# Performance work log

Hardware: AMD Instinct MI355X
Metric: run time of the kernel (lower is better)

The kernel has to match this reference:

```python
import jax, jax.numpy as jnp
import numpy as np

B, S, D, H = 2, 2048, 1024, 16
HD = D // H  # head_dim = 64


def setup_inputs() -> dict:
    key = jax.random.key(0)
    ks = jax.random.split(key, 11)
    init = 1.0 / np.sqrt(D)
    inp = {
        "query": jax.random.normal(ks[0], (B, S, D), jnp.float32),
        "key": jax.random.normal(ks[1], (B, S, D), jnp.float32),
        "value": jax.random.normal(ks[2], (B, S, D), jnp.float32),
        "Wq": jax.random.uniform(ks[3], (D, D), jnp.float32, -init, init),
        "bq": jax.random.uniform(ks[4], (D,), jnp.float32, -init, init),
        "Wk": jax.random.uniform(ks[5], (D, D), jnp.float32, -init, init),
        "bk": jax.random.uniform(ks[6], (D,), jnp.float32, -init, init),
        "Wv": jax.random.uniform(ks[7], (D, D), jnp.float32, -init, init),
        "bv": jax.random.uniform(ks[8], (D,), jnp.float32, -init, init),
        "Wo": jax.random.uniform(ks[9], (D, D), jnp.float32, -init, init),
        "bo": jax.random.uniform(ks[10], (D,), jnp.float32, -init, init),
    }
    return inp


def reference(query, key, value, Wq, bq, Wk, bk, Wv, bv, Wo, bo):
    # Linear projections (torch Linear: x @ W.T + b)
    q = query @ Wq.T + bq  # [B,S,D]
    k = key @ Wk.T + bk
    v = value @ Wv.T + bv
    # split heads -> [B,H,S,HD]
    q = q.reshape(B, S, H, HD).transpose(0, 2, 1, 3)
    k = k.reshape(B, S, H, HD).transpose(0, 2, 1, 3)
    v = v.reshape(B, S, H, HD).transpose(0, 2, 1, 3)
    # NOTE: original code divides by scale = head_dim**-0.5, i.e. multiplies
    # scores by sqrt(head_dim). Reproduced faithfully.
    scale = HD ** (-0.5)
    scores = jnp.einsum("bhqd,bhkd->bhqk", q, k) / scale  # [B,H,S,S]
    attn = jax.nn.softmax(scores, axis=-1)
    x = jnp.einsum("bhqk,bhkd->bhqd", attn, v)  # [B,H,S,HD]
    x = x.transpose(0, 2, 1, 3).reshape(B, S, D)
    return x @ Wo.T + bo
```

## Files before the change

### kernel.cpp

```cpp
#include <hip/hip_runtime.h>
#include <stdint.h>
#include <stddef.h>

#define SCALE_LOG2E 11.541560327111707f
#define E8 4194304
#define M1 1048576

typedef __attribute__((ext_vector_type(8))) _Float16 f16x8;
typedef __attribute__((ext_vector_type(4))) _Float16 f16x4;
typedef __attribute__((ext_vector_type(4))) float f32x4;

#if __has_builtin(__builtin_amdgcn_exp2f)
#define EXP2F(x) __builtin_amdgcn_exp2f(x)
#else
#define EXP2F(x) exp2f(x)
#endif

__device__ __forceinline__ f32x4 mfma_f16(f16x8 a, f16x8 b, f32x4 c) {
  return __builtin_amdgcn_mfma_f32_16x16x32_f16(a, b, c, 0, 0, 0);
}

__device__ __forceinline__ void async16(const void* g, void* lds) {
  __builtin_amdgcn_global_load_lds(
      (const __attribute__((address_space(1))) unsigned int*)g,
      (__attribute__((address_space(3))) unsigned int*)lds, 16, 0, 0);
}

__global__ void prep_x(const float* __restrict__ q, const float* __restrict__ k,
                       const float* __restrict__ v, _Float16* __restrict__ dst) {
  const int i = blockIdx.x * 256 + threadIdx.x;
  const int z = blockIdx.y;
  const float* s = (z == 0) ? q : (z == 1) ? k : v;
  float4 x = ((const float4*)s)[i];
  f16x4 h = {(_Float16)x.x, (_Float16)x.y, (_Float16)x.z, (_Float16)x.w};
  ((f16x4*)(dst + (size_t)z * E8))[i] = h;
}

__global__ void prep_w4(const float* __restrict__ wq, const float* __restrict__ wk,
                        const float* __restrict__ wv, const float* __restrict__ wo,
                        _Float16* __restrict__ dst) {
  const int i = blockIdx.x * 256 + threadIdx.x;
  const int z = blockIdx.y;
  const float* s = (z == 0) ? wq : (z == 1) ? wk : (z == 2) ? wv : wo;
  float4 x = ((const float4*)s)[i];
  f16x4 h = {(_Float16)x.x, (_Float16)x.y, (_Float16)x.z, (_Float16)x.w};
  ((f16x4*)(dst + (size_t)z * M1))[i] = h;
}

__global__ __launch_bounds__(256) void gemm_qkv(
    const _Float16* __restrict__ Xf,
    const _Float16* __restrict__ Wf,
    const float* __restrict__ bq, const float* __restrict__ bk,
    const float* __restrict__ bv,
    _Float16* __restrict__ Of)
{
  __shared__ _Float16 LA[4096];
  __shared__ _Float16 LB[4096];
  const int z = blockIdx.z;
  const int tid = threadIdx.x;
  const int lane = tid & 63;
  const int wv = tid >> 6;
  const int wm = wv >> 1, wn = wv & 1;
  const int rl = lane & 15, qd = lane >> 4;
  const int m0 = blockIdx.y * 128, n0 = blockIdx.x * 128;

  const _Float16* A0 = Xf + (size_t)z * E8;
  const _Float16* W0 = Wf + (size_t)z * M1;
  const float* bias = (z == 0) ? bq : (z == 1) ? bk : bv;

  f32x4 acc[4][4];
#pragma unroll
  for (int i = 0; i < 4; i++)
#pragma unroll
    for (int j = 0; j < 4; j++) acc[i][j] = f32x4{0.f, 0.f, 0.f, 0.f};

  const int srow = wv * 32 + (lane >> 2);
  const int scol = (lane & 3) * 8;

  for (int k0 = 0; k0 < 1024; k0 += 32) {
    const _Float16* ga = A0 + (size_t)(m0 + srow) * 1024 + k0 + scol;
    async16(ga, &LA[wv * 1024]);
    async16(ga + 16 * 1024, &LA[wv * 1024 + 512]);
    const _Float16* gb = W0 + (size_t)(n0 + srow) * 1024 + k0 + scol;
    async16(gb, &LB[wv * 1024]);
    async16(gb + 16 * 1024, &LB[wv * 1024 + 512]);
    __syncthreads();
    f16x8 af[4], bfr[4];
#pragma unroll
    for (int i = 0; i < 4; i++) af[i] = *(const f16x8*)&LA[(wm * 64 + i * 16 + rl) * 32 + qd * 8];
#pragma unroll
    for (int j = 0; j < 4; j++) bfr[j] = *(const f16x8*)&LB[(wn * 64 + j * 16 + rl) * 32 + qd * 8];
#pragma unroll
    for (int i = 0; i < 4; i++)
#pragma unroll
      for (int j = 0; j < 4; j++) acc[i][j] = mfma_f16(af[i], bfr[j], acc[i][j]);
    __syncthreads();
  }

  if (z == 2) {
#pragma unroll
    for (int j = 0; j < 4; j++) {
      const int nn = n0 + wn * 64 + j * 16 + rl;
      const float bj = bias[nn];
      const int hh = nn >> 6, e = nn & 63;
#pragma unroll
      for (int i = 0; i < 4; i++) {
        const int mm = m0 + wm * 64 + i * 16 + qd * 4;
        const int b = mm >> 11, s = mm & 2047;
        f16x4 pk = {(_Float16)(acc[i][j][0] + bj), (_Float16)(acc[i][j][1] + bj),
                    (_Float16)(acc[i][j][2] + bj), (_Float16)(acc[i][j][3] + bj)};
        *(f16x4*)(Of + 2 * (size_t)E8 + (((size_t)((b * 16 + hh) * 64 + e)) << 11) + s) = pk;
      }
    }
  } else {
    const float scl = (z == 0) ? SCALE_LOG2E : 1.0f;
    _Float16* base = Of + (size_t)z * E8;
#pragma unroll
    for (int j = 0; j < 4; j++) {
      const int nn = n0 + wn * 64 + j * 16 + rl;
      const float bj = bias[nn];
      const int hh = nn >> 6, e = nn & 63;
#pragma unroll
      for (int i = 0; i < 4; i++) {
        const int mm = m0 + wm * 64 + i * 16 + qd * 4;
        const int b = mm >> 11;
#pragma unroll
        for (int r = 0; r < 4; r++) {
          const int s = (mm + r) & 2047;
          base[((size_t)((b * 16 + hh) * 2048 + s) << 6) + e] =
              (_Float16)((acc[i][j][r] + bj) * scl);
        }
      }
    }
  }
}

__global__ __launch_bounds__(256, 2) void attn_kernel(
    const _Float16* __restrict__ Qb,
    const _Float16* __restrict__ Kb,
    const _Float16* __restrict__ Vt,
    _Float16* __restrict__ Xo)
{
  __shared__ _Float16 Ks[2][4096];
  __shared__ _Float16 Vs[2][4096];
  __shared__ _Float16 Ps[4][32][76];
  const int tid = threadIdx.x;
  const int lane = tid & 63;
  const int wv = tid >> 6;
  const int rl = lane & 15, qd = lane >> 4;
  const int bh = blockIdx.y;
  const int q0 = blockIdx.x * 128 + wv * 32;

  f16x8 qf[2][2];
#pragma unroll
  for (int mt = 0; mt < 2; mt++)
#pragma unroll
    for (int kk = 0; kk < 2; kk++)
      qf[mt][kk] = *(const f16x8*)(Qb + ((size_t)bh * 2048 + q0 + mt * 16 + rl) * 64 +
                                   kk * 32 + qd * 8);

  float m_[2] = {-1e30f, -1e30f}, l_[2] = {0.f, 0.f};
  f32x4 o[2][4];
#pragma unroll
  for (int mt = 0; mt < 2; mt++)
#pragma unroll
    for (int jt = 0; jt < 4; jt++) o[mt][jt] = f32x4{0.f, 0.f, 0.f, 0.f};

  auto stage = [&](int kv, int buf) {
#pragma unroll
    for (int it = 0; it < 2; it++) {
      const int cI = it * 256 + tid;
      const int row = cI >> 3;
      const int c = (cI & 7) ^ (row & 7);
      const int dst = (it * 256 + wv * 64) * 8;
      async16(Kb + ((size_t)bh * 2048 + kv + row) * 64 + c * 8, &Ks[buf][dst]);
      async16(Vt + ((size_t)bh * 64 + row) * 2048 + kv + c * 8, &Vs[buf][dst]);
    }
  };

  stage(0, 0);

  for (int t = 0; t < 32; t++) {
    const int buf = t & 1;
    __syncthreads();
    if (t + 1 < 32) stage((t + 1) * 64, buf ^ 1);

    f32x4 sc[2][4];
#pragma unroll
    for (int mt = 0; mt < 2; mt++)
#pragma unroll
      for (int nt = 0; nt < 4; nt++) sc[mt][nt] = f32x4{0.f, 0.f, 0.f, 0.f};
#pragma unroll
    for (int nt = 0; nt < 4; nt++) {
      const int ro = (nt * 16 + rl) * 64;
#pragma unroll
      for (int kk = 0; kk < 2; kk++) {
        const int cc = (((kk * 4 + qd) ^ (rl & 7)) << 3);
        f16x8 kh = *(const f16x8*)&Ks[buf][ro + cc];
#pragma unroll
        for (int mt = 0; mt < 2; mt++)
          sc[mt][nt] = mfma_f16(kh, qf[mt][kk], sc[mt][nt]);
      }
    }

#pragma unroll
    for (int mt = 0; mt < 2; mt++) {
      float mx = sc[mt][0][0];
#pragma unroll
      for (int nt = 0; nt < 4; nt++)
#pragma unroll
        for (int r = 0; r < 4; r++) mx = fmaxf(mx, sc[mt][nt][r]);
      mx = fmaxf(mx, __shfl_xor(mx, 16));
      mx = fmaxf(mx, __shfl_xor(mx, 32));
      const float mold = m_[mt];
      const float mnew = fmaxf(mold, mx);
      m_[mt] = mnew;
      float sm = 0.f;
#pragma unroll
      for (int nt = 0; nt < 4; nt++)
#pragma unroll
        for (int r = 0; r < 4; r++) {
          float p = EXP2F(sc[mt][nt][r] - mnew);
          sc[mt][nt][r] = p;
          sm += p;
        }
      sm += __shfl_xor(sm, 16);
      sm += __shfl_xor(sm, 32);
      if (__any(mnew > mold)) {
        const float al = EXP2F(mold - mnew);
        l_[mt] = l_[mt] * al + sm;
#pragma unroll
        for (int jt = 0; jt < 4; jt++)
#pragma unroll
          for (int r = 0; r < 4; r++) o[mt][jt][r] *= al;
      } else {
        l_[mt] += sm;
      }

#pragma unroll
      for (int nt = 0; nt < 4; nt++) {
        f16x4 pk = {(_Float16)sc[mt][nt][0], (_Float16)sc[mt][nt][1],
                    (_Float16)sc[mt][nt][2], (_Float16)sc[mt][nt][3]};
        *(f16x4*)&Ps[wv][mt * 16 + rl][nt * 16 + qd * 4] = pk;
      }
    }

#pragma unroll
    for (int kk2 = 0; kk2 < 2; kk2++) {
      f16x8 pf[2];
#pragma unroll
      for (int mt = 0; mt < 2; mt++)
        pf[mt] = *(const f16x8*)&Ps[wv][mt * 16 + rl][kk2 * 32 + qd * 8];
#pragma unroll
      for (int jt = 0; jt < 4; jt++) {
        const int cc = (((kk2 * 4 + qd) ^ (rl & 7)) << 3);
        f16x8 vv = *(const f16x8*)&Vs[buf][(jt * 16 + rl) * 64 + cc];
#pragma unroll
        for (int mt = 0; mt < 2; mt++)
          o[mt][jt] = mfma_f16(vv, pf[mt], o[mt][jt]);
      }
    }
  }

  const int b = bh >> 4, hh = bh & 15;
#pragma unroll
  for (int mt = 0; mt < 2; mt++) {
    const float inv = 1.0f / l_[mt];
    const int q = q0 + mt * 16 + rl;
#pragma unroll
    for (int jt = 0; jt < 4; jt++) {
      f16x4 pk = {(_Float16)(o[mt][jt][0] * inv), (_Float16)(o[mt][jt][1] * inv),
                  (_Float16)(o[mt][jt][2] * inv), (_Float16)(o[mt][jt][3] * inv)};
      *(f16x4*)(Xo + ((size_t)(b * 2048 + q)) * 1024 + hh * 64 + jt * 16 + qd * 4) = pk;
    }
  }
}

__global__ __launch_bounds__(256) void gemm_out(
    const _Float16* __restrict__ A0,
    const _Float16* __restrict__ W0,
    const float* __restrict__ bias,
    float* __restrict__ out)
{
  __shared__ _Float16 LA[4096];
  __shared__ _Float16 LB[4096];
  const int tid = threadIdx.x;
  const int lane = tid & 63;
  const int wv = tid >> 6;
  const int wm = wv >> 1, wn = wv & 1;
  const int rl = lane & 15, qd = lane >> 4;
  const int m0 = blockIdx.y * 128, n0 = blockIdx.x * 128;

  f32x4 acc[4][4];
#pragma unroll
  for (int i = 0; i < 4; i++)
#pragma unroll
    for (int j = 0; j < 4; j++) acc[i][j] = f32x4{0.f, 0.f, 0.f, 0.f};

  const int srow = wv * 32 + (lane >> 2);
  const int scol = (lane & 3) * 8;

  for (int k0 = 0; k0 < 1024; k0 += 32) {
    const _Float16* ga = A0 + (size_t)(m0 + srow) * 1024 + k0 + scol;
    async16(ga, &LA[wv * 1024]);
    async16(ga + 16 * 1024, &LA[wv * 1024 + 512]);
    const _Float16* gb = W0 + (size_t)(n0 + srow) * 1024 + k0 + scol;
    async16(gb, &LB[wv * 1024]);
    async16(gb + 16 * 1024, &LB[wv * 1024 + 512]);
    __syncthreads();
    f16x8 af[4], bfr[4];
#pragma unroll
    for (int i = 0; i < 4; i++) af[i] = *(const f16x8*)&LA[(wm * 64 + i * 16 + rl) * 32 + qd * 8];
#pragma unroll
    for (int j = 0; j < 4; j++) bfr[j] = *(const f16x8*)&LB[(wn * 64 + j * 16 + rl) * 32 + qd * 8];
#pragma unroll
    for (int i = 0; i < 4; i++)
#pragma unroll
      for (int j = 0; j < 4; j++) acc[i][j] = mfma_f16(af[i], bfr[j], acc[i][j]);
    __syncthreads();
  }

#pragma unroll
  for (int j = 0; j < 4; j++) {
    const int nn = n0 + wn * 64 + j * 16 + rl;
    const float bj = bias[nn];
#pragma unroll
    for (int i = 0; i < 4; i++) {
      const int mm = m0 + wm * 64 + i * 16 + qd * 4;
#pragma unroll
      for (int r = 0; r < 4; r++)
        out[(size_t)(mm + r) * 1024 + nn] = acc[i][j][r] + bj;
    }
  }
}

extern "C" void kernel_launch(void* const* d_in, const int* in_sizes, int n_in,
                              void* d_out, int out_size, void* d_ws, size_t ws_size,
                              hipStream_t stream) {
  const float* query = (const float*)d_in[0];
  const float* key   = (const float*)d_in[1];
  const float* value = (const float*)d_in[2];
  const float* Wq = (const float*)d_in[3];
  const float* bq = (const float*)d_in[4];
  const float* Wk = (const float*)d_in[5];
  const float* bk = (const float*)d_in[6];
  const float* Wv = (const float*)d_in[7];
  const float* bv = (const float*)d_in[8];
  const float* Wo = (const float*)d_in[9];
  const float* bo = (const float*)d_in[10];

  _Float16* ws = (_Float16*)d_ws;
  _Float16* Xf = ws;
  _Float16* Wf = ws + 3 * (size_t)E8;
  _Float16* Qh = Wf + 4 * (size_t)M1;
  _Float16* Kh = Qh + (size_t)E8;
  _Float16* Vt = Kh + (size_t)E8;
  _Float16* Xa = Vt + (size_t)E8;

  prep_x<<<dim3(4096, 3), 256, 0, stream>>>(query, key, value, Xf);
  prep_w4<<<dim3(1024, 4), 256, 0, stream>>>(Wq, Wk, Wv, Wo, Wf);

  gemm_qkv<<<dim3(8, 32, 3), 256, 0, stream>>>(Xf, Wf, bq, bk, bv, Qh);
  attn_kernel<<<dim3(16, 32), 256, 0, stream>>>(Qh, Kh, Vt, Xa);
  gemm_out<<<dim3(8, 32), 256, 0, stream>>>(Xa, Wf + 3 * (size_t)M1, bo, (float*)d_out);
}
```

Measured before the change: 259.7 us.

## Double-buffer GEMMs, halve attention and out-proj tiles, merge prep kernels

Merges the two fp16 conversion kernels into one launch. Adds double-buffered LDS staging with a single barrier per k-step to both GEMMs. Halves the attention query tile per wave (16 rows), which doubles the grid, and switches to a per-lane local-max softmax with the row sum reduced only at the end. Shrinks the output-projection M tile to 64 so more blocks run. The aim is to hide global-load latency and raise occupancy and block count. The cost is more K/V reloads per query in attention and somewhat different fp16 rounding of the probabilities.

```diff
diff --git a/kernel.cpp b/kernel.cpp
--- a/kernel.cpp
+++ b/kernel.cpp
@@ -26,36 +26,41 @@
       (__attribute__((address_space(3))) unsigned int*)lds, 16, 0, 0);
 }
 
-__global__ void prep_x(const float* __restrict__ q, const float* __restrict__ k,
-                       const float* __restrict__ v, _Float16* __restrict__ dst) {
-  const int i = blockIdx.x * 256 + threadIdx.x;
-  const int z = blockIdx.y;
-  const float* s = (z == 0) ? q : (z == 1) ? k : v;
-  float4 x = ((const float4*)s)[i];
+__global__ void prep_all(const float* __restrict__ q, const float* __restrict__ k,
+                         const float* __restrict__ v,
+                         const float* __restrict__ wq, const float* __restrict__ wk,
+                         const float* __restrict__ wv, const float* __restrict__ wo,
+                         _Float16* __restrict__ Xf, _Float16* __restrict__ Wf) {
+  const int gid = blockIdx.x;
+  const float* src;
+  _Float16* dst;
+  int i;
+  if (gid < 12288) {
+    const int z = gid >> 12;
+    src = (z == 0) ? q : (z == 1) ? k : v;
+    dst = Xf + (size_t)z * E8;
+    i = (gid & 4095) * 256 + threadIdx.x;
+  } else {
+    const int g2 = gid - 12288;
+    const int z = g2 >> 10;
+    src = (z == 0) ? wq : (z == 1) ? wk : (z == 2) ? wv : wo;
+    dst = Wf + (size_t)z * M1;
+    i = (g2 & 1023) * 256 + threadIdx.x;
+  }
+  float4 x = ((const float4*)src)[i];
   f16x4 h = {(_Float16)x.x, (_Float16)x.y, (_Float16)x.z, (_Float16)x.w};
-  ((f16x4*)(dst + (size_t)z * E8))[i] = h;
-}
-
-__global__ void prep_w4(const float* __restrict__ wq, const float* __restrict__ wk,
-                        const float* __restrict__ wv, const float* __restrict__ wo,
-                        _Float16* __restrict__ dst) {
-  const int i = blockIdx.x * 256 + threadIdx.x;
-  const int z = blockIdx.y;
-  const float* s = (z == 0) ? wq : (z == 1) ? wk : (z == 2) ? wv : wo;
-  float4 x = ((const float4*)s)[i];
-  f16x4 h = {(_Float16)x.x, (_Float16)x.y, (_Float16)x.z, (_Float16)x.w};
-  ((f16x4*)(dst + (size_t)z * M1))[i] = h;
-}
-
-__global__ __launch_bounds__(256) void gemm_qkv(
+  ((f16x4*)dst)[i] = h;
+}
+
+__global__ __launch_bounds__(256, 3) void gemm_qkv(
     const _Float16* __restrict__ Xf,
     const _Float16* __restrict__ Wf,
     const float* __restrict__ bq, const float* __restrict__ bk,
     const float* __restrict__ bv,
     _Float16* __restrict__ Of)
 {
-  __shared__ _Float16 LA[4096];
-  __shared__ _Float16 LB[4096];
+  __shared__ _Float16 LA[2][4096];
+  __shared__ _Float16 LB[2][4096];
   const int z = blockIdx.z;
   const int tid = threadIdx.x;
   const int lane = tid & 63;
@@ -77,24 +82,29 @@
   const int srow = wv * 32 + (lane >> 2);
   const int scol = (lane & 3) * 8;
 
-  for (int k0 = 0; k0 < 1024; k0 += 32) {
+  auto stage = [&](int k0, int buf) {
     const _Float16* ga = A0 + (size_t)(m0 + srow) * 1024 + k0 + scol;
-    async16(ga, &LA[wv * 1024]);
-    async16(ga + 16 * 1024, &LA[wv * 1024 + 512]);
+    async16(ga, &LA[buf][wv * 1024]);
+    async16(ga + 16 * 1024, &LA[buf][wv * 1024 + 512]);
     const _Float16* gb = W0 + (size_t)(n0 + srow) * 1024 + k0 + scol;
-    async16(gb, &LB[wv * 1024]);
-    async16(gb + 16 * 1024, &LB[wv * 1024 + 512]);
+    async16(gb, &LB[buf][wv * 1024]);
+    async16(gb + 16 * 1024, &LB[buf][wv * 1024 + 512]);
+  };
+
+  stage(0, 0);
+  for (int t = 0; t < 32; t++) {
+    const int buf = t & 1;
     __syncthreads();
+    if (t + 1 < 32) stage((t + 1) * 32, buf ^ 1);
     f16x8 af[4], bfr[4];
 #pragma unroll
-    for (int i = 0; i < 4; i++) af[i] = *(const f16x8*)&LA[(wm * 64 + i * 16 + rl) * 32 + qd * 8];
-#pragma unroll
-    for (int j = 0; j < 4; j++) bfr[j] = *(const f16x8*)&LB[(wn * 64 + j * 16 + rl) * 32 + qd * 8];
+    for (int i = 0; i < 4; i++) af[i] = *(const f16x8*)&LA[buf][(wm * 64 + i * 16 + rl) * 32 + qd * 8];
+#pragma unroll
+    for (int j = 0; j < 4; j++) bfr[j] = *(const f16x8*)&LB[buf][(wn * 64 + j * 16 + rl) * 32 + qd * 8];
 #pragma unroll
     for (int i = 0; i < 4; i++)
 #pragma unroll
       for (int j = 0; j < 4; j++) acc[i][j] = mfma_f16(af[i], bfr[j], acc[i][j]);
-    __syncthreads();
   }
 
   if (z == 2) {
@@ -135,7 +145,7 @@
   }
 }
 
-__global__ __launch_bounds__(256, 2) void attn_kernel(
+__global__ __launch_bounds__(256, 3) void attn_kernel(
     const _Float16* __restrict__ Qb,
     const _Float16* __restrict__ Kb,
     const _Float16* __restrict__ Vt,
@@ -143,28 +153,23 @@
 {
   __shared__ _Float16 Ks[2][4096];
   __shared__ _Float16 Vs[2][4096];
-  __shared__ _Float16 Ps[4][32][76];
+  __shared__ _Float16 Ps[4][16][76];
   const int tid = threadIdx.x;
   const int lane = tid & 63;
   const int wv = tid >> 6;
   const int rl = lane & 15, qd = lane >> 4;
   const int bh = blockIdx.y;
-  const int q0 = blockIdx.x * 128 + wv * 32;
-
-  f16x8 qf[2][2];
-#pragma unroll
-  for (int mt = 0; mt < 2; mt++)
-#pragma unroll
-    for (int kk = 0; kk < 2; kk++)
-      qf[mt][kk] = *(const f16x8*)(Qb + ((size_t)bh * 2048 + q0 + mt * 16 + rl) * 64 +
-                                   kk * 32 + qd * 8);
-
-  float m_[2] = {-1e30f, -1e30f}, l_[2] = {0.f, 0.f};
-  f32x4 o[2][4];
-#pragma unroll
-  for (int mt = 0; mt < 2; mt++)
-#pragma unroll
-    for (int jt = 0; jt < 4; jt++) o[mt][jt] = f32x4{0.f, 0.f, 0.f, 0.f};
+  const int q0 = blockIdx.x * 64 + wv * 16;
+
+  f16x8 qf[2];
+#pragma unroll
+  for (int kk = 0; kk < 2; kk++)
+    qf[kk] = *(const f16x8*)(Qb + ((size_t)bh * 2048 + q0 + rl) * 64 + kk * 32 + qd * 8);
+
+  float m_ = -1e30f, l_ = 0.f;
+  f32x4 o[4];
+#pragma unroll
+  for (int jt = 0; jt < 4; jt++) o[jt] = f32x4{0.f, 0.f, 0.f, 0.f};
 
   auto stage = [&](int kv, int buf) {
 #pragma unroll
@@ -185,11 +190,9 @@
     __syncthreads();
     if (t + 1 < 32) stage((t + 1) * 64, buf ^ 1);
 
-    f32x4 sc[2][4];
-#pragma unroll
-    for (int mt = 0; mt < 2; mt++)
-#pragma unroll
-      for (int nt = 0; nt < 4; nt++) sc[mt][nt] = f32x4{0.f, 0.f, 0.f, 0.f};
+    f32x4 sc[4];
+#pragma unroll
+    for (int nt = 0; nt < 4; nt++) sc[nt] = f32x4{0.f, 0.f, 0.f, 0.f};
 #pragma unroll
     for (int nt = 0; nt < 4; nt++) {
       const int ro = (nt * 16 + rl) * 64;
@@ -197,127 +200,122 @@
       for (int kk = 0; kk < 2; kk++) {
         const int cc = (((kk * 4 + qd) ^ (rl & 7)) << 3);
         f16x8 kh = *(const f16x8*)&Ks[buf][ro + cc];
-#pragma unroll
-        for (int mt = 0; mt < 2; mt++)
-          sc[mt][nt] = mfma_f16(kh, qf[mt][kk], sc[mt][nt]);
-      }
-    }
-
-#pragma unroll
-    for (int mt = 0; mt < 2; mt++) {
-      float mx = sc[mt][0][0];
-#pragma unroll
-      for (int nt = 0; nt < 4; nt++)
-#pragma unroll
-        for (int r = 0; r < 4; r++) mx = fmaxf(mx, sc[mt][nt][r]);
-      mx = fmaxf(mx, __shfl_xor(mx, 16));
-      mx = fmaxf(mx, __shfl_xor(mx, 32));
-      const float mold = m_[mt];
-      const float mnew = fmaxf(mold, mx);
-      m_[mt] = mnew;
-      float sm = 0.f;
-#pragma unroll
-      for (int nt = 0; nt < 4; nt++)
-#pragma unroll
-        for (int r = 0; r < 4; r++) {
-          float p = EXP2F(sc[mt][nt][r] - mnew);
-          sc[mt][nt][r] = p;
-          sm += p;
-        }
-      sm += __shfl_xor(sm, 16);
-      sm += __shfl_xor(sm, 32);
-      if (__any(mnew > mold)) {
-        const float al = EXP2F(mold - mnew);
-        l_[mt] = l_[mt] * al + sm;
-#pragma unroll
-        for (int jt = 0; jt < 4; jt++)
-#pragma unroll
-          for (int r = 0; r < 4; r++) o[mt][jt][r] *= al;
-      } else {
-        l_[mt] += sm;
-      }
-
-#pragma unroll
-      for (int nt = 0; nt < 4; nt++) {
-        f16x4 pk = {(_Float16)sc[mt][nt][0], (_Float16)sc[mt][nt][1],
-                    (_Float16)sc[mt][nt][2], (_Float16)sc[mt][nt][3]};
-        *(f16x4*)&Ps[wv][mt * 16 + rl][nt * 16 + qd * 4] = pk;
-      }
+        sc[nt] = mfma_f16(kh, qf[kk], sc[nt]);
+      }
+    }
+
+    float mloc = sc[0][0];
+#pragma unroll
+    for (int nt = 0; nt < 4; nt++)
+#pragma unroll
+      for (int r = 0; r < 4; r++) mloc = fmaxf(mloc, sc[nt][r]);
+    float mx = fmaxf(mloc, __shfl_xor(mloc, 16));
+    mx = fmaxf(mx, __shfl_xor(mx, 32));
+    float sm = 0.f;
+#pragma unroll
+    for (int nt = 0; nt < 4; nt++)
+#pragma unroll
+      for (int r = 0; r < 4; r++) {
+        float p = EXP2F(sc[nt][r] - mloc);
+        sc[nt][r] = p;
+        sm += p;
+      }
+    const float mold = m_;
+    const float mnew = fmaxf(mold, mx);
+    m_ = mnew;
+    const float cf = EXP2F(mloc - mnew);
+    if (__any(mnew > mold)) {
+      const float al = EXP2F(mold - mnew);
+      l_ = l_ * al + sm * cf;
+#pragma unroll
+      for (int jt = 0; jt < 4; jt++)
+#pragma unroll
+        for (int r = 0; r < 4; r++) o[jt][r] *= al;
+    } else {
+      l_ += sm * cf;
+    }
+
+#pragma unroll
+    for (int nt = 0; nt < 4; nt++) {
+      f16x4 pk = {(_Float16)(sc[nt][0] * cf), (_Float16)(sc[nt][1] * cf),
+                  (_Float16)(sc[nt][2] * cf), (_Float16)(sc[nt][3] * cf)};
+      *(f16x4*)&Ps[wv][rl][nt * 16 + qd * 4] = pk;
     }
 
 #pragma unroll
     for (int kk2 = 0; kk2 < 2; kk2++) {
-      f16x8 pf[2];
-#pragma unroll
-      for (int mt = 0; mt < 2; mt++)
-        pf[mt] = *(const f16x8*)&Ps[wv][mt * 16 + rl][kk2 * 32 + qd * 8];
+      f16x8 pf = *(const f16x8*)&Ps[wv][rl][kk2 * 32 + qd * 8];
 #pragma unroll
       for (int jt = 0; jt < 4; jt++) {
         const int cc = (((kk2 * 4 + qd) ^ (rl & 7)) << 3);
         f16x8 vv = *(const f16x8*)&Vs[buf][(jt * 16 + rl) * 64 + cc];
-#pragma unroll
-        for (int mt = 0; mt < 2; mt++)
-          o[mt][jt] = mfma_f16(vv, pf[mt], o[mt][jt]);
-      }
-    }
-  }
-
+        o[jt] = mfma_f16(vv, pf, o[jt]);
+      }
+    }
+  }
+
+  float lt = l_ + __shfl_xor(l_, 16);
+  lt += __shfl_xor(lt, 32);
+  const float inv = 1.0f / lt;
   const int b = bh >> 4, hh = bh & 15;
-#pragma unroll
-  for (int mt = 0; mt < 2; mt++) {
-    const float inv = 1.0f / l_[mt];
-    const int q = q0 + mt * 16 + rl;
-#pragma unroll
-    for (int jt = 0; jt < 4; jt++) {
-      f16x4 pk = {(_Float16)(o[mt][jt][0] * inv), (_Float16)(o[mt][jt][1] * inv),
-                  (_Float16)(o[mt][jt][2] * inv), (_Float16)(o[mt][jt][3] * inv)};
-      *(f16x4*)(Xo + ((size_t)(b * 2048 + q)) * 1024 + hh * 64 + jt * 16 + qd * 4) = pk;
-    }
-  }
-}
-
-__global__ __launch_bounds__(256) void gemm_out(
+  const int q = q0 + rl;
+#pragma unroll
+  for (int jt = 0; jt < 4; jt++) {
+    f16x4 pk = {(_Float16)(o[jt][0] * inv), (_Float16)(o[jt][1] * inv),
+                (_Float16)(o[jt][2] * inv), (_Float16)(o[jt][3] * inv)};
+    *(f16x4*)(Xo + ((size_t)(b * 2048 + q)) * 1024 + hh * 64 + jt * 16 + qd * 4) = pk;
+  }
+}
+
+__global__ __launch_bounds__(256, 2) void gemm_out(
     const _Float16* __restrict__ A0,
     const _Float16* __restrict__ W0,
     const float* __restrict__ bias,
     float* __restrict__ out)
 {
-  __shared__ _Float16 LA[4096];
-  __shared__ _Float16 LB[4096];
+  __shared__ _Float16 LA[2][2048];
+  __shared__ _Float16 LB[2][4096];
   const int tid = threadIdx.x;
   const int lane = tid & 63;
   const int wv = tid >> 6;
   const int wm = wv >> 1, wn = wv & 1;
   const int rl = lane & 15, qd = lane >> 4;
-  const int m0 = blockIdx.y * 128, n0 = blockIdx.x * 128;
-
-  f32x4 acc[4][4];
-#pragma unroll
-  for (int i = 0; i < 4; i++)
+  const int m0 = blockIdx.y * 64, n0 = blockIdx.x * 128;
+
+  f32x4 acc[2][4];
+#pragma unroll
+  for (int i = 0; i < 2; i++)
 #pragma unroll
     for (int j = 0; j < 4; j++) acc[i][j] = f32x4{0.f, 0.f, 0.f, 0.f};
 
-  const int srow = wv * 32 + (lane >> 2);
-  const int scol = (lane & 3) * 8;
-
-  for (int k0 = 0; k0 < 1024; k0 += 32) {
-    const _Float16* ga = A0 + (size_t)(m0 + srow) * 1024 + k0 + scol;
-    async16(ga, &LA[wv * 1024]);
-    async16(ga + 16 * 1024, &LA[wv * 1024 + 512]);
-    const _Float16* gb = W0 + (size_t)(n0 + srow) * 1024 + k0 + scol;
-    async16(gb, &LB[wv * 1024]);
-    async16(gb + 16 * 1024, &LB[wv * 1024 + 512]);
+  auto stage = [&](int k0, int buf) {
+    {
+      const int row = tid >> 2, c = tid & 3;
+      async16(A0 + (size_t)(m0 + row) * 1024 + k0 + c * 8, &LA[buf][wv * 512]);
+    }
+#pragma unroll
+    for (int it = 0; it < 2; it++) {
+      const int cI = it * 256 + tid;
+      const int row = cI >> 2, c = cI & 3;
+      async16(W0 + (size_t)(n0 + row) * 1024 + k0 + c * 8,
+              &LB[buf][it * 2048 + wv * 512]);
+    }
+  };
+
+  stage(0, 0);
+  for (int t = 0; t < 32; t++) {
+    const int buf = t & 1;
     __syncthreads();
-    f16x8 af[4], bfr[4];
-#pragma unroll
-    for (int i = 0; i < 4; i++) af[i] = *(const f16x8*)&LA[(wm * 64 + i * 16 + rl) * 32 + qd * 8];
-#pragma unroll
-    for (int j = 0; j < 4; j++) bfr[j] = *(const f16x8*)&LB[(wn * 64 + j * 16 + rl) * 32 + qd * 8];
-#pragma unroll
-    for (int i = 0; i < 4; i++)
+    if (t + 1 < 32) stage((t + 1) * 32, buf ^ 1);
+    f16x8 af[2], bfr[4];
+#pragma unroll
+    for (int i = 0; i < 2; i++) af[i] = *(const f16x8*)&LA[buf][(wm * 32 + i * 16 + rl) * 32 + qd * 8];
+#pragma unroll
+    for (int j = 0; j < 4; j++) bfr[j] = *(const f16x8*)&LB[buf][(wn * 64 + j * 16 + rl) * 32 + qd * 8];
+#pragma unroll
+    for (int i = 0; i < 2; i++)
 #pragma unroll
       for (int j = 0; j < 4; j++) acc[i][j] = mfma_f16(af[i], bfr[j], acc[i][j]);
-    __syncthreads();
   }
 
 #pragma unroll
@@ -325,8 +323,8 @@
     const int nn = n0 + wn * 64 + j * 16 + rl;
     const float bj = bias[nn];
 #pragma unroll
-    for (int i = 0; i < 4; i++) {
-      const int mm = m0 + wm * 64 + i * 16 + qd * 4;
+    for (int i = 0; i < 2; i++) {
+      const int mm = m0 + wm * 32 + i * 16 + qd * 4;
 #pragma unroll
       for (int r = 0; r < 4; r++)
         out[(size_t)(mm + r) * 1024 + nn] = acc[i][j][r] + bj;
@@ -357,10 +355,8 @@
   _Float16* Vt = Kh + (size_t)E8;
   _Float16* Xa = Vt + (size_t)E8;
 
-  prep_x<<<dim3(4096, 3), 256, 0, stream>>>(query, key, value, Xf);
-  prep_w4<<<dim3(1024, 4), 256, 0, stream>>>(Wq, Wk, Wv, Wo, Wf);
-
+  prep_all<<<16384, 256, 0, stream>>>(query, key, value, Wq, Wk, Wv, Wo, Xf, Wf);
   gemm_qkv<<<dim3(8, 32, 3), 256, 0, stream>>>(Xf, Wf, bq, bk, bv, Qh);
-  attn_kernel<<<dim3(16, 32), 256, 0, stream>>>(Qh, Kh, Vt, Xa);
-  gemm_out<<<dim3(8, 32), 256, 0, stream>>>(Xa, Wf + 3 * (size_t)M1, bo, (float*)d_out);
-}
+  attn_kernel<<<dim3(32, 32), 256, 0, stream>>>(Qh, Kh, Vt, Xa);
+  gemm_out<<<dim3(8, 64), 256, 0, stream>>>(Xa, Wf + 3 * (size_t)M1, bo, (float*)d_out);
+}
```

Measured after the change: 254.6 us. No clear change (-2.0%).
